# Kernel tuning notes

Hardware: AMD Instinct MI355X
Metric: run time of the kernel (lower is better)

Reference implementation:

```python
import jax, jax.numpy as jnp
import numpy as np

EPS = 1e-5
N, M, ORIG, NBR, F, H, N0 = 100000, 12, 92, 41, 64, 128, 2000


def _bn(x, gamma, beta):
    # BatchNorm1d in training mode: biased batch stats over axis 0
    mu = jnp.mean(x, axis=0)
    var = jnp.var(x, axis=0)
    return (x - mu) * jax.lax.rsqrt(var + EPS) * gamma + beta


def _conv_layer(a, nbr, idx, W, b, g1, bt1, g2, bt2):
    n, m = idx.shape
    f = a.shape[1]
    a_nbr = a[idx]  # (N, M, F) gather
    tot = jnp.concatenate(
        [jnp.broadcast_to(a[:, None, :], (n, m, f)), a_nbr, nbr], axis=2
    )  # (N, M, 2F + nbr_fea_len)
    gated = (tot @ W + b).reshape(n * m, 2 * f)
    gated = _bn(gated, g1, bt1).reshape(n, m, 2 * f)
    filt, core = jnp.split(gated, 2, axis=2)
    summed = jnp.sum(jax.nn.sigmoid(filt) * jax.nn.softplus(core), axis=1)  # (N, F)
    summed = _bn(summed, g2, bt2)
    return jax.nn.softplus(a + summed)


def setup_inputs() -> dict:
    key = jax.random.key(0)
    ks = jax.random.split(key, 24)
    s = lambda shape, k, scale=0.05: jax.random.normal(k, shape, jnp.float32) * scale
    inp = {
        "atom_fea": jax.random.normal(ks[0], (N, ORIG), jnp.float32),
        "nbr_fea": jax.random.normal(ks[1], (N, M, NBR), jnp.float32),
        "nbr_fea_idx": jax.random.randint(ks[2], (N, M), 0, N),
        "crystal_id": jnp.sort(jax.random.randint(ks[3], (N,), 0, N0)),
        # embedding
        "W_emb": s((ORIG, F), ks[4]), "b_emb": s((F,), ks[5]),
        # conv layer
        "cW": s((2 * F + NBR, 2 * F), ks[6]), "cb": s((2 * F,), ks[7]),
        "cg1": jnp.ones((2 * F,), jnp.float32), "cbt1": jnp.zeros((2 * F,), jnp.float32),
        "cg2": jnp.ones((F,), jnp.float32), "cbt2": jnp.zeros((F,), jnp.float32),
        # residual block conv layer
        "rW": s((2 * F + NBR, 2 * F), ks[8]), "rb": s((2 * F,), ks[9]),
        "rg1": jnp.ones((2 * F,), jnp.float32), "rbt1": jnp.zeros((2 * F,), jnp.float32),
        "rg2": jnp.ones((F,), jnp.float32), "rbt2": jnp.zeros((F,), jnp.float32),
        # head
        "W_fc": s((F, H), ks[10]), "b_fc": s((H,), ks[11]),
        "W_out": s((H, 1), ks[12]), "b_out": s((1,), ks[13]),
    }
    return inp


def reference(atom_fea, nbr_fea, nbr_fea_idx, crystal_id,
              W_emb, b_emb, cW, cb, cg1, cbt1, cg2, cbt2,
              rW, rb, rg1, rbt1, rg2, rbt2, W_fc, b_fc, W_out, b_out):
    a = atom_fea @ W_emb + b_emb  # (N, F)
    a1 = _conv_layer(a, nbr_fea, nbr_fea_idx, cW, cb, cg1, cbt1, cg2, cbt2)
    # Res_block: softplus(conv(a1) + a1)
    a2 = jax.nn.softplus(
        _conv_layer(a1, nbr_fea, nbr_fea_idx, rW, rb, rg1, rbt1, rg2, rbt2) + a1
    )
    # per-crystal mean pooling (segment mean)
    cnt = jax.ops.segment_sum(jnp.ones((a2.shape[0],), a2.dtype), crystal_id, N0)
    crys = jax.ops.segment_sum(a2, crystal_id, N0) / jnp.maximum(cnt, 1.0)[:, None]
    crys = jax.nn.softplus(jax.nn.softplus(crys) @ W_fc + b_fc)
    return crys @ W_out + b_out  # (N0, 1)
```

## Files before the change

kernel.cpp:

```cpp
#include <hip/hip_runtime.h>
#include <hip/hip_bf16.h>

namespace {

constexpr int N    = 100000;
constexpr int M    = 12;
constexpr int ORIG = 92;
constexpr int NBR  = 41;
constexpr int F    = 64;
constexpr int H    = 128;
constexpr int N0   = 2000;
constexpr float EPS = 1e-5f;

constexpr int NBLK2 = N / 32;

typedef __attribute__((ext_vector_type(8))) short bf16x8;
typedef __attribute__((ext_vector_type(4))) float f32x4;
typedef float f32x4u __attribute__((ext_vector_type(4), aligned(4)));

__device__ __forceinline__ float u2f(unsigned u){ float f; __builtin_memcpy(&f, &u, 4); return f; }

__device__ __forceinline__ float softplusf(float x){
  float t = __expf(-fabsf(x));
  return fmaxf(x, 0.f) + 0.693147180559945f * __log2f(1.f + t);
}
__device__ __forceinline__ float sigmoidf(float x){
  return __fdividef(1.f, 1.f + __expf(-x));
}
__device__ __forceinline__ unsigned short f2bf(float f){
  __hip_bfloat16 h = __float2bfloat16(f);
  unsigned short u; __builtin_memcpy(&u, &h, 2); return u;
}
__device__ __forceinline__ unsigned packbf2(float lo, float hi){
  __hip_bfloat162 b2 = __float22bfloat162_rn(make_float2(lo, hi));
  unsigned u; __builtin_memcpy(&u, &b2, 4); return u;
}
__device__ __forceinline__ void cvt2(bf16x8& d, int e, float a, float b){
  unsigned u = packbf2(a, b);
  d[e]   = (short)(u & 0xffffu);
  d[e+1] = (short)(u >> 16);
}

__global__ void k_embed(const float* __restrict__ af, const float* __restrict__ W,
                        const float* __restrict__ b, float* __restrict__ a){
  __shared__ float row[4][ORIG];
  int base = blockIdx.x * 4;
  for(int t = threadIdx.x; t < 4*ORIG; t += 256){
    row[t/ORIG][t%ORIG] = af[(size_t)(base + t/ORIG)*ORIG + (t%ORIG)];
  }
  __syncthreads();
  int i = base + (threadIdx.x >> 6);
  int j = threadIdx.x & 63;
  const float* r = row[threadIdx.x >> 6];
  float acc = b[j];
  #pragma unroll
  for(int k = 0; k < ORIG; k++) acc = fmaf(r[k], W[k*F + j], acc);
  a[(size_t)i*F + j] = acc;
}

__global__ void k_nbrcvt(const float* __restrict__ nbr, unsigned short* __restrict__ NB){
  const long long total = (long long)N*M*6;
  long long stride = (long long)gridDim.x * blockDim.x;
  for(long long c = (long long)blockIdx.x*blockDim.x + threadIdx.x; c < total; c += stride){
    int seg = (int)(c % 6);
    long long row = c / 6;
    const float* src = nbr + row*NBR + seg*8;
    bf16x8 o = {0,0,0,0,0,0,0,0};
    if(seg < 5){
      f32x4u v0 = *(const f32x4u*)src;
      f32x4u v1 = *(const f32x4u*)(src + 4);
      cvt2(o, 0, v0.x, v0.y); cvt2(o, 2, v0.z, v0.w);
      cvt2(o, 4, v1.x, v1.y); cvt2(o, 6, v1.z, v1.w);
    } else {
      o[0] = (short)f2bf(src[0]);
    }
    *(bf16x8*)(NB + c*8) = o;
  }
}

__global__ void k_prep(const float* __restrict__ W,
                       unsigned short* __restrict__ webf,
                       unsigned short* __restrict__ wspf){
  int b = blockIdx.x;
  int l = threadIdx.x, lr = l & 15, lg = l >> 4;
  if(b < 16){
    int ct = b >> 1, s = b & 1;
    unsigned short* dst = webf + ((size_t)b*64 + l)*8;
    #pragma unroll
    for(int e = 0; e < 8; ++e){
      int k = s*32 + lg*8 + e;
      float w = (k < NBR) ? W[(size_t)(128 + k)*128 + ct*16 + lr] : 0.f;
      dst[e] = f2bf(w);
    }
  } else {
    int f = b - 16;
    int ct = f >> 1, ks = f & 1;
    int col = ct*16 + lr;
    unsigned short* dst = wspf + ((size_t)f*64 + l)*8;
    #pragma unroll
    for(int e = 0; e < 8; ++e){
      int k = ks*32 + lg*8 + e;
      float w = (col < 128) ? W[(size_t)k*128 + col]
                            : W[(size_t)(64 + k)*128 + (col - 128)];
      dst[e] = f2bf(w);
    }
  }
}

__global__ __launch_bounds__(256, 3)
void k_spmm(const float* __restrict__ X, const unsigned short* __restrict__ wspf,
            const float* __restrict__ bias,
            unsigned* __restrict__ SU, unsigned* __restrict__ P2u){
  const int tid = threadIdx.x;
  const int l = tid & 63, lr = l & 15, lg = l >> 4;
  const int w = tid >> 6;
  const int a0 = blockIdx.x * 32;
  const bf16x8* wv = (const bf16x8*)wspf;

  bf16x8 BS[2][2], BPl[2], BPh[2];
  #pragma unroll
  for(int ks = 0; ks < 2; ++ks){
    BS[0][ks] = wv[((w)*2 + ks)*64 + l];
    BS[1][ks] = wv[((4 + w)*2 + ks)*64 + l];
    BPl[ks]   = wv[((8 + w)*2 + ks)*64 + l];
    BPh[ks]   = wv[((12 + w)*2 + ks)*64 + l];
  }

  bf16x8 A[2][2];
  #pragma unroll
  for(int t = 0; t < 2; ++t){
    const float* xr = X + (size_t)(a0 + t*16 + lr)*64;
    #pragma unroll
    for(int ks = 0; ks < 2; ++ks){
      f32x4u v0 = *(const f32x4u*)(xr + ks*32 + lg*8);
      f32x4u v1 = *(const f32x4u*)(xr + ks*32 + lg*8 + 4);
      cvt2(A[t][ks], 0, v0.x, v0.y); cvt2(A[t][ks], 2, v0.z, v0.w);
      cvt2(A[t][ks], 4, v1.x, v1.y); cvt2(A[t][ks], 6, v1.z, v1.w);
    }
  }

  f32x4 DS[2][2], DPl[2], DPh[2];
  #pragma unroll
  for(int t = 0; t < 2; ++t){
    #pragma unroll
    for(int c = 0; c < 2; ++c){
      f32x4 z = {0.f,0.f,0.f,0.f};
      z = __builtin_amdgcn_mfma_f32_16x16x32_bf16(A[t][0], BS[c][0], z, 0, 0, 0);
      z = __builtin_amdgcn_mfma_f32_16x16x32_bf16(A[t][1], BS[c][1], z, 0, 0, 0);
      DS[t][c] = z;
    }
    f32x4 zl = {0.f,0.f,0.f,0.f}, zh = {0.f,0.f,0.f,0.f};
    zl = __builtin_amdgcn_mfma_f32_16x16x32_bf16(A[t][0], BPl[0], zl, 0, 0, 0);
    zl = __builtin_amdgcn_mfma_f32_16x16x32_bf16(A[t][1], BPl[1], zl, 0, 0, 0);
    zh = __builtin_amdgcn_mfma_f32_16x16x32_bf16(A[t][0], BPh[0], zh, 0, 0, 0);
    zh = __builtin_amdgcn_mfma_f32_16x16x32_bf16(A[t][1], BPh[1], zh, 0, 0, 0);
    DPl[t] = zl; DPh[t] = zh;
  }

  float b0 = bias[w*16 + lr], b1 = bias[64 + w*16 + lr];

  #pragma unroll
  for(int t = 0; t < 2; ++t){
    #pragma unroll
    for(int r = 0; r < 4; ++r){
      size_t row = a0 + t*16 + lg*4 + r;
      SU[row*64 + w*16 + lr]  = packbf2(DS[t][0][r] + b0, DS[t][1][r] + b1);
      P2u[row*64 + w*16 + lr] = packbf2(DPl[t][r], DPh[t][r]);
    }
  }
}

template<int MODE, int NBF>
__global__ __launch_bounds__(256, 4)
void k_pass2(const unsigned* __restrict__ SU, const unsigned* __restrict__ P2u,
             const float* __restrict__ nbr, const unsigned short* __restrict__ NB,
             const int* __restrict__ idx, const unsigned short* __restrict__ webf,
             const float* __restrict__ sc1, const float* __restrict__ sh1,
             float* __restrict__ SUMb, float* __restrict__ part){
  const int tid = threadIdx.x;
  const int l = tid & 63, lr = l & 15, lg = l >> 4;
  const int wid = tid >> 6, tw = wid >> 1, h = wid & 1;
  const int a0 = blockIdx.x*32 + tw*16;

  bf16x8 Bf[4][2];
  const bf16x8* wv = (const bf16x8*)webf;
  #pragma unroll
  for(int c = 0; c < 4; ++c){
    int cg = (c < 2) ? (2*h + c) : (4 + 2*h + (c - 2));
    Bf[c][0] = wv[(cg*2 + 0)*64 + l];
    Bf[c][1] = wv[(cg*2 + 1)*64 + l];
  }

  unsigned SDu[2][4];
  #pragma unroll
  for(int fc = 0; fc < 2; ++fc)
    #pragma unroll
    for(int r = 0; r < 4; ++r)
      SDu[fc][r] = SU[(size_t)(a0 + lg*4 + r)*64 + h*32 + fc*16 + lr];

  __shared__ int six[32*M];
  for(int u = tid; u < 32*M; u += 256) six[u] = idx[(size_t)blockIdx.x*32*M + u];
  __syncthreads();

  float c1f[2], h1f[2], c1c[2], h1c[2];
  if(MODE == 1){
    #pragma unroll
    for(int fc = 0; fc < 2; ++fc){
      int j = h*32 + fc*16 + lr;
      c1f[fc] = sc1[j];      h1f[fc] = sh1[j];
      c1c[fc] = sc1[64 + j]; h1c[fc] = sh1[64 + j];
    }
  }

  float sg[4] = {0,0,0,0}, ssg[4] = {0,0,0,0};
  float sact[4][2];
  #pragma unroll
  for(int r = 0; r < 4; ++r){ sact[r][0] = 0.f; sact[r][1] = 0.f; }

  const unsigned short* nbase;
  const float* fbase;
  if constexpr(NBF) nbase = NB + (size_t)(a0 + lr)*M*48;
  else              fbase = nbr + (size_t)(a0 + lr)*M*NBR;

  #define LOAD_A(mm, A0o, A1o)                                              \
    do{                                                                     \
      if constexpr(NBF){                                                    \
        const unsigned short* nrow = nbase + (size_t)(mm)*48;               \
        A0o = *(const bf16x8*)(nrow + lg*8);                                \
        if(lg < 2) A1o = *(const bf16x8*)(nrow + 32 + lg*8);                \
        else       A1o = (bf16x8){0,0,0,0,0,0,0,0};                         \
      } else {                                                              \
        const float* nrow = fbase + (size_t)(mm)*NBR;                       \
        f32x4u v0 = *(const f32x4u*)(nrow + lg*8);                          \
        f32x4u v1 = *(const f32x4u*)(nrow + lg*8 + 4);                      \
        cvt2(A0o, 0, v0.x, v0.y); cvt2(A0o, 2, v0.z, v0.w);                 \
        cvt2(A0o, 4, v1.x, v1.y); cvt2(A0o, 6, v1.z, v1.w);                 \
        A1o = (bf16x8){0,0,0,0,0,0,0,0};                                    \
        if(lg == 0){                                                        \
          f32x4u w0 = *(const f32x4u*)(nrow + 32);                          \
          f32x4u w1 = *(const f32x4u*)(nrow + 36);                          \
          cvt2(A1o, 0, w0.x, w0.y); cvt2(A1o, 2, w0.z, w0.w);               \
          cvt2(A1o, 4, w1.x, w1.y); cvt2(A1o, 6, w1.z, w1.w);               \
        } else if(lg == 1){                                                 \
          A1o[0] = (short)f2bf(nrow[40]);                                   \
        }                                                                   \
      }                                                                     \
    }while(0)

  bf16x8 cA0, cA1, nA0, nA1;
  LOAD_A(0, cA0, cA1);

  #pragma unroll 1
  for(int m = 0; m < M; ++m){
    if(m + 1 < M) LOAD_A(m + 1, nA0, nA1);

    f32x4 D[4];
    #pragma unroll
    for(int c = 0; c < 4; ++c){
      f32x4 z = {0.f,0.f,0.f,0.f};
      z = __builtin_amdgcn_mfma_f32_16x16x32_bf16(cA0, Bf[c][0], z, 0, 0, 0);
      z = __builtin_amdgcn_mfma_f32_16x16x32_bf16(cA1, Bf[c][1], z, 0, 0, 0);
      D[c] = z;
    }

    #pragma unroll
    for(int r = 0; r < 4; ++r){
      int p = six[(tw*16 + lg*4 + r)*M + m];
      const unsigned* Prow = P2u + (size_t)p*64 + h*32 + lr;
      #pragma unroll
      for(int fc = 0; fc < 2; ++fc){
        unsigned pv = Prow[fc*16];
        unsigned sv = SDu[fc][r];
        float gf = D[fc][r]     + u2f(sv << 16)         + u2f(pv << 16);
        float gc = D[2 + fc][r] + u2f(sv & 0xffff0000u) + u2f(pv & 0xffff0000u);
        if(MODE == 0){
          sg[fc]     += gf;  ssg[fc]     = fmaf(gf, gf, ssg[fc]);
          sg[2 + fc] += gc;  ssg[2 + fc] = fmaf(gc, gc, ssg[2 + fc]);
        } else {
          float bf_ = fmaf(gf, c1f[fc], h1f[fc]);
          float bc_ = fmaf(gc, c1c[fc], h1c[fc]);
          sact[r][fc] += sigmoidf(bf_) * softplusf(bc_);
        }
      }
    }
    cA0 = nA0; cA1 = nA1;
  }
  #undef LOAD_A

  if(MODE == 0){
    #pragma unroll
    for(int c = 0; c < 4; ++c){
      sg[c]  += __shfl_xor(sg[c], 16, 64);  sg[c]  += __shfl_xor(sg[c], 32, 64);
      ssg[c] += __shfl_xor(ssg[c], 16, 64); ssg[c] += __shfl_xor(ssg[c], 32, 64);
    }
    if(lg == 0){
      float* pb = part + ((size_t)blockIdx.x*2 + tw)*256;
      #pragma unroll
      for(int c = 0; c < 4; ++c){
        int col = (c < 2) ? (h*32 + c*16 + lr) : (64 + h*32 + (c - 2)*16 + lr);
        pb[col]       = sg[c];
        pb[128 + col] = ssg[c];
      }
    }
  } else {
    float ps[2] = {0,0}, pss[2] = {0,0};
    #pragma unroll
    for(int fc = 0; fc < 2; ++fc){
      #pragma unroll
      for(int r = 0; r < 4; ++r){
        float v = sact[r][fc];
        SUMb[(size_t)(a0 + lg*4 + r)*64 + h*32 + fc*16 + lr] = v;
        ps[fc] += v; pss[fc] = fmaf(v, v, pss[fc]);
      }
      ps[fc]  += __shfl_xor(ps[fc], 16, 64);  ps[fc]  += __shfl_xor(ps[fc], 32, 64);
      pss[fc] += __shfl_xor(pss[fc], 16, 64); pss[fc] += __shfl_xor(pss[fc], 32, 64);
    }
    if(lg == 0){
      float* pb = part + ((size_t)blockIdx.x*2 + tw)*128;
      #pragma unroll
      for(int fc = 0; fc < 2; ++fc){
        int j = h*32 + fc*16 + lr;
        pb[j]      = ps[fc];
        pb[64 + j] = pss[fc];
      }
    }
  }
}

__global__ void k_reduce(const float* __restrict__ part, int nblocks, int width,
                         float* __restrict__ out){
  int col = blockIdx.x;
  float s = 0.f;
  for(int b = threadIdx.x; b < nblocks; b += 256) s += part[(size_t)b*width + col];
  __shared__ float red[256];
  red[threadIdx.x] = s;
  __syncthreads();
  for(int off = 128; off; off >>= 1){
    if(threadIdx.x < off) red[threadIdx.x] += red[threadIdx.x + off];
    __syncthreads();
  }
  if(threadIdx.x == 0) out[col] = red[0];
}

__global__ void k_finalize(const float* __restrict__ red, const float* __restrict__ gamma,
                           const float* __restrict__ beta, float* __restrict__ sc,
                           float* __restrict__ sh, float inv, int nch){
  int j = threadIdx.x;
  if(j < nch){
    float mu  = red[j] * inv;
    float var = fmaxf(red[nch + j] * inv - mu*mu, 0.f);
    float r   = rsqrtf(var + EPS);
    float s   = gamma[j] * r;
    sc[j] = s;
    sh[j] = beta[j] - mu * s;
  }
}

__global__ void k_epi(const float* __restrict__ X, const float* __restrict__ SUMb,
                      const float* __restrict__ sc2, const float* __restrict__ sh2,
                      float* __restrict__ Y, int res){
  int stride = gridDim.x * blockDim.x;
  int total = N*F/4;
  for(int e4 = blockIdx.x * blockDim.x + threadIdx.x; e4 < total; e4 += stride){
    f32x4 x = *(const f32x4*)(X + (size_t)e4*4);
    f32x4 s = *(const f32x4*)(SUMb + (size_t)e4*4);
    int j0 = (e4*4) & 63;
    f32x4 y;
    #pragma unroll
    for(int u = 0; u < 4; ++u){
      float t = softplusf(x[u] + fmaf(s[u], sc2[j0 + u], sh2[j0 + u]));
      y[u] = res ? softplusf(t + x[u]) : t;
    }
    *(f32x4*)(Y + (size_t)e4*4) = y;
  }
}

__global__ void k_pool(const float* __restrict__ A2, const int* __restrict__ cid,
                       float* __restrict__ POOL){
  int c = blockIdx.x;
  int j = threadIdx.x;
  int lo = 0, hi = N;
  while(lo < hi){ int mid = (lo + hi) >> 1; if(cid[mid] < c) lo = mid + 1; else hi = mid; }
  int s0 = lo;
  lo = s0; hi = N;
  while(lo < hi){ int mid = (lo + hi) >> 1; if(cid[mid] < c + 1) lo = mid + 1; else hi = mid; }
  int s1 = lo;
  float s = 0.f;
  for(int i = s0; i < s1; i++) s += A2[(size_t)i*F + j];
  POOL[c*F + j] = s / fmaxf((float)(s1 - s0), 1.f);
}

__global__ void k_head(const float* __restrict__ POOL, const float* __restrict__ Wfc,
                       const float* __restrict__ bfc, const float* __restrict__ Wout,
                       const float* __restrict__ bout, float* __restrict__ out){
  int c = blockIdx.x;
  int t = threadIdx.x;
  __shared__ float spv[F];
  if(t < F) spv[t] = softplusf(POOL[c*F + t]);
  __syncthreads();
  float h = bfc[t];
  #pragma unroll
  for(int k = 0; k < F; k++) h = fmaf(spv[k], Wfc[k*H + t], h);
  h = softplusf(h);
  float v = h * Wout[t];
  #pragma unroll
  for(int off = 32; off; off >>= 1) v += __shfl_down(v, off, 64);
  __shared__ float red[2];
  if((t & 63) == 0) red[t >> 6] = v;
  __syncthreads();
  if(t == 0) out[c] = red[0] + red[1] + bout[0];
}

constexpr size_t OFF_A0   = 0;
constexpr size_t OFF_A1   = 25600000;
constexpr size_t OFF_SUMB = 51200000;
constexpr size_t OFF_SU   = 76800000;
constexpr size_t OFF_P2U  = 102400000;
constexpr size_t OFF_POOL = 128000000;
constexpr size_t OFF_SP1  = 128512000;
constexpr size_t OFF_SP2  = 134912000;
constexpr size_t OFF_STAT = 138112000;
constexpr size_t OFF_WEBF = 138120192;
constexpr size_t OFF_WSPF = 138136576;
constexpr size_t OFF_NB   = 138169344;
constexpr size_t WS_NEED_NB = OFF_NB + (size_t)N*M*48*2;

}

extern "C" void kernel_launch(void* const* d_in, const int* in_sizes, int n_in,
                              void* d_out, int out_size, void* d_ws, size_t ws_size,
                              hipStream_t stream){
  const float* atom_fea = (const float*)d_in[0];
  const float* nbr_fea  = (const float*)d_in[1];
  const int*   nbr_idx  = (const int*)d_in[2];
  const int*   cid      = (const int*)d_in[3];
  const float* W_emb = (const float*)d_in[4];
  const float* b_emb = (const float*)d_in[5];
  const float* cW  = (const float*)d_in[6];
  const float* cb  = (const float*)d_in[7];
  const float* cg1 = (const float*)d_in[8];
  const float* cbt1= (const float*)d_in[9];
  const float* cg2 = (const float*)d_in[10];
  const float* cbt2= (const float*)d_in[11];
  const float* rW  = (const float*)d_in[12];
  const float* rb  = (const float*)d_in[13];
  const float* rg1 = (const float*)d_in[14];
  const float* rbt1= (const float*)d_in[15];
  const float* rg2 = (const float*)d_in[16];
  const float* rbt2= (const float*)d_in[17];
  const float* W_fc = (const float*)d_in[18];
  const float* b_fc = (const float*)d_in[19];
  const float* W_out= (const float*)d_in[20];
  const float* b_out= (const float*)d_in[21];
  float* out = (float*)d_out;

  char* ws = (char*)d_ws;
  float*    A0   = (float*)(ws + OFF_A0);
  float*    A1   = (float*)(ws + OFF_A1);
  float*    SUMb = (float*)(ws + OFF_SUMB);
  unsigned* SU   = (unsigned*)(ws + OFF_SU);
  unsigned* P2u  = (unsigned*)(ws + OFF_P2U);
  float*    POOL = (float*)(ws + OFF_POOL);
  float*    SP1  = (float*)(ws + OFF_SP1);
  float*    SP2  = (float*)(ws + OFF_SP2);
  float*    STAT = (float*)(ws + OFF_STAT);
  unsigned short* WEBf = (unsigned short*)(ws + OFF_WEBF);
  unsigned short* WSPf = (unsigned short*)(ws + OFF_WSPF);
  unsigned short* NB   = (unsigned short*)(ws + OFF_NB);
  float* RED1 = STAT;
  float* RED2 = STAT + 256;
  float* SC1  = STAT + 384;
  float* SH1  = STAT + 512;
  float* SC2  = STAT + 640;
  float* SH2  = STAT + 704;

  const bool use_nb = (ws_size >= WS_NEED_NB);

  k_embed<<<N/4, 256, 0, stream>>>(atom_fea, W_emb, b_emb, A0);
  if(use_nb) k_nbrcvt<<<2048, 256, 0, stream>>>(nbr_fea, NB);

  for(int layer = 0; layer < 2; layer++){
    const float* W   = layer ? rW   : cW;
    const float* bb  = layer ? rb   : cb;
    const float* g1  = layer ? rg1  : cg1;
    const float* bt1 = layer ? rbt1 : cbt1;
    const float* g2  = layer ? rg2  : cg2;
    const float* bt2 = layer ? rbt2 : cbt2;
    const float* X = layer ? A1 : A0;
    float*       Y = layer ? A0 : A1;

    k_prep<<<48, 64, 0, stream>>>(W, WEBf, WSPf);
    k_spmm<<<NBLK2, 256, 0, stream>>>(X, WSPf, bb, SU, P2u);
    if(use_nb){
      k_pass2<0,1><<<NBLK2, 256, 0, stream>>>(SU, P2u, nbr_fea, NB, nbr_idx,
                                              WEBf, SC1, SH1, nullptr, SP1);
    } else {
      k_pass2<0,0><<<NBLK2, 256, 0, stream>>>(SU, P2u, nbr_fea, nullptr, nbr_idx,
                                              WEBf, SC1, SH1, nullptr, SP1);
    }
    k_reduce<<<256, 256, 0, stream>>>(SP1, 2*NBLK2, 256, RED1);
    k_finalize<<<1, 128, 0, stream>>>(RED1, g1, bt1, SC1, SH1, 1.f/(float)(N*M), 128);
    if(use_nb){
      k_pass2<1,1><<<NBLK2, 256, 0, stream>>>(SU, P2u, nbr_fea, NB, nbr_idx,
                                              WEBf, SC1, SH1, SUMb, SP2);
    } else {
      k_pass2<1,0><<<NBLK2, 256, 0, stream>>>(SU, P2u, nbr_fea, nullptr, nbr_idx,
                                              WEBf, SC1, SH1, SUMb, SP2);
    }
    k_reduce<<<128, 256, 0, stream>>>(SP2, 2*NBLK2, 128, RED2);
    k_finalize<<<1, 128, 0, stream>>>(RED2, g2, bt2, SC2, SH2, 1.f/(float)N, 64);
    k_epi<<<2048, 256, 0, stream>>>(X, SUMb, SC2, SH2, Y, layer);
  }

  k_pool<<<N0, 64, 0, stream>>>(A0, cid, POOL);
  k_head<<<N0, 128, 0, stream>>>(POOL, W_fc, b_fc, W_out, b_out, out);
}
```

Before: 634.0 us.

## Tile-interleave bf16 neighbor features and pack gathered projections into 64-bit words

The bf16 copy of the neighbor features is reordered into 16-atom tiles laid out by neighbor slot, so each MFMA A-operand load for one neighbor slot reads a contiguous 1.5 KB block instead of rows strided by M. The neighbor projection buffer is repacked so each lane's two filter/core values for a gathered atom sit in one 64-bit word. This turns two scattered 32-bit gather loads into one wider load. The spmm kernel is rebalanced so two waves produce the self term and two produce the packed neighbor term.

After: 634.7 us. About the same (+0.1%).

```diff
diff --git a/kernel.cpp b/kernel.cpp
--- a/kernel.cpp
+++ b/kernel.cpp
@@ -59,12 +59,16 @@
 }
 
 __global__ void k_nbrcvt(const float* __restrict__ nbr, unsigned short* __restrict__ NB){
-  const long long total = (long long)N*M*6;
+  const long long total = (long long)(N/16)*M*16*6;
   long long stride = (long long)gridDim.x * blockDim.x;
   for(long long c = (long long)blockIdx.x*blockDim.x + threadIdx.x; c < total; c += stride){
     int seg = (int)(c % 6);
-    long long row = c / 6;
-    const float* src = nbr + row*NBR + seg*8;
+    long long t3 = c / 6;
+    int r = (int)(t3 % 16);
+    long long t4 = t3 / 16;
+    int m = (int)(t4 % M);
+    long long atile = t4 / M;
+    const float* src = nbr + (((size_t)(atile*16 + r)*M + m)*NBR) + seg*8;
     bf16x8 o = {0,0,0,0,0,0,0,0};
     if(seg < 5){
       f32x4u v0 = *(const f32x4u*)src;
@@ -110,22 +114,13 @@
 __global__ __launch_bounds__(256, 3)
 void k_spmm(const float* __restrict__ X, const unsigned short* __restrict__ wspf,
             const float* __restrict__ bias,
-            unsigned* __restrict__ SU, unsigned* __restrict__ P2u){
+            unsigned* __restrict__ SU, unsigned long long* __restrict__ Q){
   const int tid = threadIdx.x;
   const int l = tid & 63, lr = l & 15, lg = l >> 4;
   const int w = tid >> 6;
   const int a0 = blockIdx.x * 32;
   const bf16x8* wv = (const bf16x8*)wspf;
 
-  bf16x8 BS[2][2], BPl[2], BPh[2];
-  #pragma unroll
-  for(int ks = 0; ks < 2; ++ks){
-    BS[0][ks] = wv[((w)*2 + ks)*64 + l];
-    BS[1][ks] = wv[((4 + w)*2 + ks)*64 + l];
-    BPl[ks]   = wv[((8 + w)*2 + ks)*64 + l];
-    BPh[ks]   = wv[((12 + w)*2 + ks)*64 + l];
-  }
-
   bf16x8 A[2][2];
   #pragma unroll
   for(int t = 0; t < 2; ++t){
@@ -139,40 +134,63 @@
     }
   }
 
-  f32x4 DS[2][2], DPl[2], DPh[2];
-  #pragma unroll
-  for(int t = 0; t < 2; ++t){
-    #pragma unroll
-    for(int c = 0; c < 2; ++c){
+  const bool isS = (w < 2);
+  const int hh = isS ? w : (w - 2);
+  int tl[4];
+  if(isS){ tl[0] = 2*w; tl[1] = 2*w + 1; tl[2] = 4 + 2*w; tl[3] = 5 + 2*w; }
+  else   { tl[0] = 8 + 2*hh; tl[1] = 9 + 2*hh; tl[2] = 12 + 2*hh; tl[3] = 13 + 2*hh; }
+
+  bf16x8 B[4][2];
+  #pragma unroll
+  for(int ct = 0; ct < 4; ++ct)
+    #pragma unroll
+    for(int ks = 0; ks < 2; ++ks)
+      B[ct][ks] = wv[((size_t)tl[ct]*2 + ks)*64 + l];
+
+  f32x4 D[2][4];
+  #pragma unroll
+  for(int t = 0; t < 2; ++t)
+    #pragma unroll
+    for(int ct = 0; ct < 4; ++ct){
       f32x4 z = {0.f,0.f,0.f,0.f};
-      z = __builtin_amdgcn_mfma_f32_16x16x32_bf16(A[t][0], BS[c][0], z, 0, 0, 0);
-      z = __builtin_amdgcn_mfma_f32_16x16x32_bf16(A[t][1], BS[c][1], z, 0, 0, 0);
-      DS[t][c] = z;
-    }
-    f32x4 zl = {0.f,0.f,0.f,0.f}, zh = {0.f,0.f,0.f,0.f};
-    zl = __builtin_amdgcn_mfma_f32_16x16x32_bf16(A[t][0], BPl[0], zl, 0, 0, 0);
-    zl = __builtin_amdgcn_mfma_f32_16x16x32_bf16(A[t][1], BPl[1], zl, 0, 0, 0);
-    zh = __builtin_amdgcn_mfma_f32_16x16x32_bf16(A[t][0], BPh[0], zh, 0, 0, 0);
-    zh = __builtin_amdgcn_mfma_f32_16x16x32_bf16(A[t][1], BPh[1], zh, 0, 0, 0);
-    DPl[t] = zl; DPh[t] = zh;
-  }
-
-  float b0 = bias[w*16 + lr], b1 = bias[64 + w*16 + lr];
-
-  #pragma unroll
-  for(int t = 0; t < 2; ++t){
-    #pragma unroll
-    for(int r = 0; r < 4; ++r){
-      size_t row = a0 + t*16 + lg*4 + r;
-      SU[row*64 + w*16 + lr]  = packbf2(DS[t][0][r] + b0, DS[t][1][r] + b1);
-      P2u[row*64 + w*16 + lr] = packbf2(DPl[t][r], DPh[t][r]);
-    }
+      z = __builtin_amdgcn_mfma_f32_16x16x32_bf16(A[t][0], B[ct][0], z, 0, 0, 0);
+      z = __builtin_amdgcn_mfma_f32_16x16x32_bf16(A[t][1], B[ct][1], z, 0, 0, 0);
+      D[t][ct] = z;
+    }
+
+  if(isS){
+    float blo[2], bhi[2];
+    #pragma unroll
+    for(int ct = 0; ct < 2; ++ct){
+      blo[ct] = bias[32*w + ct*16 + lr];
+      bhi[ct] = bias[64 + 32*w + ct*16 + lr];
+    }
+    #pragma unroll
+    for(int t = 0; t < 2; ++t)
+      #pragma unroll
+      for(int r = 0; r < 4; ++r){
+        size_t row = a0 + t*16 + lg*4 + r;
+        #pragma unroll
+        for(int ct = 0; ct < 2; ++ct)
+          SU[row*64 + 32*w + ct*16 + lr] =
+            packbf2(D[t][ct][r] + blo[ct], D[t][2 + ct][r] + bhi[ct]);
+      }
+  } else {
+    #pragma unroll
+    for(int t = 0; t < 2; ++t)
+      #pragma unroll
+      for(int r = 0; r < 4; ++r){
+        size_t row = a0 + t*16 + lg*4 + r;
+        unsigned p0 = packbf2(D[t][0][r], D[t][2][r]);
+        unsigned p1 = packbf2(D[t][1][r], D[t][3][r]);
+        Q[row*32 + hh*16 + lr] = ((unsigned long long)p1 << 32) | p0;
+      }
   }
 }
 
 template<int MODE, int NBF>
 __global__ __launch_bounds__(256, 4)
-void k_pass2(const unsigned* __restrict__ SU, const unsigned* __restrict__ P2u,
+void k_pass2(const unsigned* __restrict__ SU, const unsigned long long* __restrict__ Q,
              const float* __restrict__ nbr, const unsigned short* __restrict__ NB,
              const int* __restrict__ idx, const unsigned short* __restrict__ webf,
              const float* __restrict__ sc1, const float* __restrict__ sh1,
@@ -217,15 +235,15 @@
   #pragma unroll
   for(int r = 0; r < 4; ++r){ sact[r][0] = 0.f; sact[r][1] = 0.f; }
 
-  const unsigned short* nbase;
+  const unsigned short* nb_tile;
   const float* fbase;
-  if constexpr(NBF) nbase = NB + (size_t)(a0 + lr)*M*48;
+  if constexpr(NBF) nb_tile = NB + (size_t)(blockIdx.x*2 + tw)*M*768;
   else              fbase = nbr + (size_t)(a0 + lr)*M*NBR;
 
   #define LOAD_A(mm, A0o, A1o)                                              \
     do{                                                                     \
       if constexpr(NBF){                                                    \
-        const unsigned short* nrow = nbase + (size_t)(mm)*48;               \
+        const unsigned short* nrow = nb_tile + (size_t)(mm)*768 + lr*48;    \
         A0o = *(const bf16x8*)(nrow + lg*8);                                \
         if(lg < 2) A1o = *(const bf16x8*)(nrow + 32 + lg*8);                \
         else       A1o = (bf16x8){0,0,0,0,0,0,0,0};                         \
@@ -266,10 +284,13 @@
     #pragma unroll
     for(int r = 0; r < 4; ++r){
       int p = six[(tw*16 + lg*4 + r)*M + m];
-      const unsigned* Prow = P2u + (size_t)p*64 + h*32 + lr;
+      unsigned long long q = Q[(size_t)p*32 + h*16 + lr];
+      unsigned pvs[2];
+      pvs[0] = (unsigned)(q & 0xffffffffull);
+      pvs[1] = (unsigned)(q >> 32);
       #pragma unroll
       for(int fc = 0; fc < 2; ++fc){
-        unsigned pv = Prow[fc*16];
+        unsigned pv = pvs[fc];
         unsigned sv = SDu[fc][r];
         float gf = D[fc][r]     + u2f(sv << 16)         + u2f(pv << 16);
         float gc = D[2 + fc][r] + u2f(sv & 0xffff0000u) + u2f(pv & 0xffff0000u);
@@ -415,7 +436,7 @@
 constexpr size_t OFF_A1   = 25600000;
 constexpr size_t OFF_SUMB = 51200000;
 constexpr size_t OFF_SU   = 76800000;
-constexpr size_t OFF_P2U  = 102400000;
+constexpr size_t OFF_Q    = 102400000;
 constexpr size_t OFF_POOL = 128000000;
 constexpr size_t OFF_SP1  = 128512000;
 constexpr size_t OFF_SP2  = 134912000;
@@ -459,7 +480,7 @@
   float*    A1   = (float*)(ws + OFF_A1);
   float*    SUMb = (float*)(ws + OFF_SUMB);
   unsigned* SU   = (unsigned*)(ws + OFF_SU);
-  unsigned* P2u  = (unsigned*)(ws + OFF_P2U);
+  unsigned long long* Q = (unsigned long long*)(ws + OFF_Q);
   float*    POOL = (float*)(ws + OFF_POOL);
   float*    SP1  = (float*)(ws + OFF_SP1);
   float*    SP2  = (float*)(ws + OFF_SP2);
@@ -490,21 +511,21 @@
     float*       Y = layer ? A0 : A1;
 
     k_prep<<<48, 64, 0, stream>>>(W, WEBf, WSPf);
-    k_spmm<<<NBLK2, 256, 0, stream>>>(X, WSPf, bb, SU, P2u);
+    k_spmm<<<NBLK2, 256, 0, stream>>>(X, WSPf, bb, SU, Q);
     if(use_nb){
-      k_pass2<0,1><<<NBLK2, 256, 0, stream>>>(SU, P2u, nbr_fea, NB, nbr_idx,
+      k_pass2<0,1><<<NBLK2, 256, 0, stream>>>(SU, Q, nbr_fea, NB, nbr_idx,
                                               WEBf, SC1, SH1, nullptr, SP1);
     } else {
-      k_pass2<0,0><<<NBLK2, 256, 0, stream>>>(SU, P2u, nbr_fea, nullptr, nbr_idx,
+      k_pass2<0,0><<<NBLK2, 256, 0, stream>>>(SU, Q, nbr_fea, nullptr, nbr_idx,
                                               WEBf, SC1, SH1, nullptr, SP1);
     }
     k_reduce<<<256, 256, 0, stream>>>(SP1, 2*NBLK2, 256, RED1);
     k_finalize<<<1, 128, 0, stream>>>(RED1, g1, bt1, SC1, SH1, 1.f/(float)(N*M), 128);
     if(use_nb){
-      k_pass2<1,1><<<NBLK2, 256, 0, stream>>>(SU, P2u, nbr_fea, NB, nbr_idx,
+      k_pass2<1,1><<<NBLK2, 256, 0, stream>>>(SU, Q, nbr_fea, NB, nbr_idx,
                                               WEBf, SC1, SH1, SUMb, SP2);
     } else {
-      k_pass2<1,0><<<NBLK2, 256, 0, stream>>>(SU, P2u, nbr_fea, nullptr, nbr_idx,
+      k_pass2<1,0><<<NBLK2, 256, 0, stream>>>(SU, Q, nbr_fea, nullptr, nbr_idx,
                                               WEBf, SC1, SH1, SUMb, SP2);
     }
     k_reduce<<<128, 256, 0, stream>>>(SP2, 2*NBLK2, 128, RED2);
```
